# Performance work log

Hardware: AMD Instinct MI355X
Metric: run time of the kernel (lower is better)

Reference implementation:

```python
import jax, jax.numpy as jnp
import numpy as np
import math

B = 2
L = 2048
D_MODEL = 1024
D_STATE = 16
D_CONV = 4
D_INNER = 2 * D_MODEL  # expand * d_model
DT_RANK = math.ceil(D_MODEL / 16)  # 64
DT_MIN, DT_MAX = 1e-3, 1e-1


def _dt_bias(k):
    # inv-softplus init of dt bias, as in Mamba
    dt = jnp.exp(jax.random.uniform(k, (D_INNER,)) * (math.log(DT_MAX) - math.log(DT_MIN)) + math.log(DT_MIN))
    dt = jnp.clip(dt, 1e-4, None)
    return (dt + jnp.log(-jnp.expm1(-dt))).astype(jnp.float32)


def setup_inputs() -> dict:
    key = jax.random.key(0)
    ks = jax.random.split(key, 14)
    nrm = lambda k, shape, s: (jax.random.normal(k, shape) * s).astype(jnp.float32)
    dt_std = DT_RANK ** -0.5
    A_log = jnp.log(jnp.broadcast_to(jnp.arange(1, D_STATE + 1, dtype=jnp.float32), (D_INNER, D_STATE)))
    return {
        "hidden_states": jax.random.normal(ks[0], (B, L, D_MODEL), dtype=jnp.float32),
        "in_proj_w": nrm(ks[1], (2 * D_INNER, D_MODEL), D_MODEL ** -0.5),
        "conv_w": nrm(ks[2], (D_INNER, D_CONV), 0.5),
        "conv_b": nrm(ks[3], (D_INNER,), 0.1),
        "x_proj_w": nrm(ks[4], (DT_RANK + 2 * D_STATE, D_INNER), D_INNER ** -0.5),
        "dt_proj_w": jax.random.uniform(ks[5], (D_INNER, DT_RANK), minval=-dt_std, maxval=dt_std).astype(jnp.float32),
        "dt_proj_b": _dt_bias(ks[6]),
        "A_log": A_log,
        "D": jnp.ones((D_INNER,), jnp.float32),
        "conv_wb": nrm(ks[7], (D_INNER, D_CONV), 0.5),
        "conv_bb": nrm(ks[8], (D_INNER,), 0.1),
        "x_proj_wb": nrm(ks[9], (DT_RANK + 2 * D_STATE, D_INNER), D_INNER ** -0.5),
        "dt_proj_wb": jax.random.uniform(ks[10], (D_INNER, DT_RANK), minval=-dt_std, maxval=dt_std).astype(jnp.float32),
        "dt_proj_bb": _dt_bias(ks[11]),
        "A_b_log": A_log,
        "D_b": jnp.ones((D_INNER,), jnp.float32),
        "out_proj_w": nrm(ks[12], (D_MODEL, D_INNER), D_INNER ** -0.5),
    }


def _causal_conv(x, w, b):
    # x: (B, d_inner, L); depthwise causal conv1d (torch pads both sides then truncates to L == left-pad d_conv-1)
    out = jax.lax.conv_general_dilated(
        x, w[:, None, :], (1,), [(D_CONV - 1, 0)],
        dimension_numbers=("NCH", "OIH", "NCH"), feature_group_count=D_INNER)
    return out + b[None, :, None]


def _selective_scan(u, dt, A, Bm, Cm, Dp, z):
    # u, dt, z: (B, d, L); A: (d, n); Bm, Cm: (B, n, L)
    h0 = jnp.zeros((u.shape[0], u.shape[1], A.shape[1]), u.dtype)

    def step(h, inp):
        dt_l, u_l, B_l, C_l = inp  # (B,d), (B,d), (B,n), (B,n)
        h = jnp.exp(dt_l[..., None] * A) * h + (dt_l * u_l)[..., None] * B_l[:, None, :]
        return h, jnp.einsum("bdn,bn->bd", h, C_l)

    xs = tuple(jnp.moveaxis(a, -1, 0) for a in (dt, u, Bm, Cm))  # time-major
    _, ys = jax.lax.scan(step, h0, xs)  # ys: (L, B, d)
    y = jnp.moveaxis(ys, 0, -1) + Dp[None, :, None] * u
    return y * jax.nn.silu(z)


def _mamba_dir(xz, conv_w, conv_b, x_proj_w, dt_proj_w, dt_proj_b, A_log, Dp):
    x, z = jnp.split(xz, 2, axis=1)  # (B, d_inner, L) each
    x = jax.nn.silu(_causal_conv(x, conv_w, conv_b))
    x_dbl = jnp.einsum("bdl,ed->bel", x, x_proj_w)  # e = dt_rank + 2*d_state
    dtv = x_dbl[:, :DT_RANK]
    Bm = x_dbl[:, DT_RANK:DT_RANK + D_STATE]
    Cm = x_dbl[:, DT_RANK + D_STATE:]
    dtv = jax.nn.softplus(jnp.einsum("brl,dr->bdl", dtv, dt_proj_w) + dt_proj_b[None, :, None])
    return _selective_scan(x, dtv, -jnp.exp(A_log), Bm, Cm, Dp, z)


def reference(hidden_states, in_proj_w, conv_w, conv_b, x_proj_w, dt_proj_w, dt_proj_b, A_log, D,
              conv_wb, conv_bb, x_proj_wb, dt_proj_wb, dt_proj_bb, A_b_log, D_b, out_proj_w):
    xz = jnp.einsum("bld,ed->bel", hidden_states, in_proj_w)  # (B, 2*d_inner, L)
    out_f = _mamba_dir(xz, conv_w, conv_b, x_proj_w, dt_proj_w, dt_proj_b, A_log, D)
    out_b = _mamba_dir(xz[..., ::-1], conv_wb, conv_bb, x_proj_wb, dt_proj_wb, dt_proj_bb, A_b_log, D_b)
    y = out_f + out_b[..., ::-1]  # (B, d_inner, L)
    return jnp.einsum("bdl,od->blo", y, out_proj_w)  # (B, L, d_model)
```

## Files before the change

### kernel.cpp

```cpp
#include <hip/hip_runtime.h>
#include <hip/hip_bf16.h>

#define B_  2
#define L_  2048
#define DM  1024
#define DI  2048
#define DS  16
#define DR  64
#define E_  4096
#define CH  32
#define NC  (L_/CH)
#define XE  128
#define KS  4
#define BLDI ((size_t)B_*L_*DI)

typedef __attribute__((ext_vector_type(8))) short bf16x8;
typedef __attribute__((ext_vector_type(4))) float f32x4;

static __device__ __forceinline__ float sigmoidf_(float x){ return 1.f/(1.f+__expf(-x)); }
static __device__ __forceinline__ float siluf_(float x){ return x*sigmoidf_(x); }
static __device__ __forceinline__ unsigned short f2bf(float f){
  unsigned int u = __float_as_uint(f);
  unsigned int r = (u + 0x7FFFu + ((u>>16)&1u)) >> 16;
  return (unsigned short)r;
}
static __device__ __forceinline__ float bf2f(unsigned short s){
  return __uint_as_float(((unsigned int)s)<<16);
}

__global__ __launch_bounds__(256) void k_prep(const float* __restrict__ hs,
                                              const float* __restrict__ wi,
                                              const float* __restrict__ wo,
                                              const float* __restrict__ wx0,
                                              const float* __restrict__ wx1,
                                              const float* __restrict__ wd0,
                                              const float* __restrict__ wd1,
                                              unsigned short* __restrict__ hsb,
                                              unsigned short* __restrict__ wib,
                                              unsigned short* __restrict__ wob,
                                              unsigned short* __restrict__ wxb0,
                                              unsigned short* __restrict__ wxb1,
                                              unsigned short* __restrict__ wdtb0,
                                              unsigned short* __restrict__ wdtb1){
  int bid = blockIdx.x;
  const float* src; unsigned short* dst; bool pad = false;
  if      (bid <  4096){ src=hs;  dst=hsb; }
  else if (bid <  8192){ bid-=4096;  src=wi;  dst=wib; }
  else if (bid < 10240){ bid-=8192;  src=wo;  dst=wob; }
  else if (bid < 10496){ bid-=10240; src=wx0; dst=wxb0; pad=true; }
  else if (bid < 10752){ bid-=10496; src=wx1; dst=wxb1; pad=true; }
  else if (bid < 10880){ bid-=10752; src=wd0; dst=wdtb0; }
  else                 { bid-=10880; src=wd1; dst=wdtb1; }
  int i = (bid*256 + threadIdx.x)*4;
  ushort4 o;
  if (pad && i >= 96*DI){ o.x=o.y=o.z=o.w=0; }
  else {
    float4 v = *(const float4*)(src + i);
    o.x = f2bf(v.x); o.y = f2bf(v.y); o.z = f2bf(v.z); o.w = f2bf(v.w);
  }
  *(ushort4*)(dst + i) = o;
}

template<int OP>
__global__ __launch_bounds__(256) void k_gemm(const unsigned short* __restrict__ A, size_t aBS, size_t aDS,
                                              const unsigned short* __restrict__ Bm, size_t bBS, size_t bDS,
                                              void* __restrict__ Cv, size_t cBS, size_t cDS,
                                              const float* __restrict__ bias0,
                                              const float* __restrict__ bias1,
                                              int K, int lda, int ldb, int ldc, int zdiv){
  __shared__ unsigned short LB[128*128];
  unsigned short* Al = LB;
  unsigned short* Bl = LB + 128*64;
  const int zz = blockIdx.z;
  const int bq = zz % zdiv, dq = zz / zdiv;
  const int m0 = blockIdx.y*128, n0 = blockIdx.x*128;
  const int tid = threadIdx.x;
  const int lane = tid & 63, wid = tid >> 6;
  const int wm = wid >> 1, wn = wid & 1;
  const unsigned short* Ab = A + (size_t)bq*aBS + (size_t)dq*aDS;
  const unsigned short* Bb = Bm + (size_t)bq*bBS + (size_t)dq*bDS;
  f32x4 acc[4][4];
  #pragma unroll
  for (int i=0;i<4;i++)
    #pragma unroll
    for (int j=0;j<4;j++){ f32x4 z = {0.f,0.f,0.f,0.f}; acc[i][j] = z; }

  for (int kt=0; kt<K; kt+=64){
    #pragma unroll
    for (int i=0;i<4;i++){
      int q = i*256 + tid;
      int row = q>>3, seg = q&7;
      int sseg = seg ^ (row&7);
      const unsigned short* ga = Ab + (size_t)(m0+row)*lda + kt + sseg*8;
      const unsigned short* gb = Bb + (size_t)(n0+row)*ldb + kt + sseg*8;
      __builtin_amdgcn_global_load_lds((const __attribute__((address_space(1))) void*)ga,
          (__attribute__((address_space(3))) void*)(Al + (size_t)q*8), 16, 0, 0);
      __builtin_amdgcn_global_load_lds((const __attribute__((address_space(1))) void*)gb,
          (__attribute__((address_space(3))) void*)(Bl + (size_t)q*8), 16, 0, 0);
    }
    __syncthreads();
    #pragma unroll
    for (int ks=0; ks<2; ks++){
      bf16x8 af[4], bfr[4];
      #pragma unroll
      for (int mf=0; mf<4; mf++){
        int row = wm*64 + mf*16 + (lane&15);
        int seg = (ks*4 + (lane>>4)) ^ (row&7);
        af[mf] = *(const bf16x8*)(Al + row*64 + seg*8);
      }
      #pragma unroll
      for (int nf=0; nf<4; nf++){
        int row = wn*64 + nf*16 + (lane&15);
        int seg = (ks*4 + (lane>>4)) ^ (row&7);
        bfr[nf] = *(const bf16x8*)(Bl + row*64 + seg*8);
      }
      #pragma unroll
      for (int mf=0; mf<4; mf++)
        #pragma unroll
        for (int nf=0; nf<4; nf++)
          acc[mf][nf] = __builtin_amdgcn_mfma_f32_16x16x32_bf16(af[mf], bfr[nf], acc[mf][nf], 0,0,0);
    }
    __syncthreads();
  }
  const float* bias = dq ? bias1 : bias0;
  if (OP==0){
    #pragma unroll
    for (int mf=0; mf<4; mf++){
      #pragma unroll
      for (int nf=0; nf<4; nf++){
        const int col   = n0 + wn*64 + nf*16 + (lane&15);
        const int rbase = m0 + wm*64 + mf*16 + (lane>>4)*4;
        #pragma unroll
        for (int r=0;r<4;r++){
          size_t o = (size_t)bq*cBS + (size_t)dq*cDS + (size_t)(rbase+r)*ldc + col;
          ((float*)Cv)[o] = acc[mf][nf][r];
        }
      }
    }
  } else {
    #pragma unroll
    for (int mf=0; mf<4; mf++){
      #pragma unroll
      for (int nf=0; nf<4; nf++){
        const int cl = wn*64 + nf*16 + (lane&15);
        const int rb = wm*64 + mf*16 + (lane>>4)*4;
        float bv = (OP==4) ? bias[n0+cl] : 0.f;
        #pragma unroll
        for (int r=0;r<4;r++){
          float v = acc[mf][nf][r];
          if (OP==5) v = siluf_(v);
          if (OP==4){ float t = v + bv; v = (t>20.f)? t : __logf(1.f+__expf(t)); }
          const int row = rb + r;
          const int sg = (cl>>3) ^ (((row>>2)&3)<<2);
          LB[row*128 + sg*8 + (cl&7)] = f2bf(v);
        }
      }
    }
    __syncthreads();
    unsigned short* Cb = (unsigned short*)Cv + (size_t)bq*cBS + (size_t)dq*cDS;
    #pragma unroll
    for (int p=0;p<8;p++){
      const int row = p*16 + (tid>>4);
      const int g = tid&15;
      const int sg = g ^ (((row>>2)&3)<<2);
      bf16x8 vv = *(const bf16x8*)&LB[row*128 + sg*8];
      *(bf16x8*)(Cb + (size_t)(m0+row)*ldc + n0 + g*8) = vv;
    }
  }
}

__global__ __launch_bounds__(256) void k_redx(const float* __restrict__ xpart,
                                              unsigned short* __restrict__ out){
  const size_t STR = (size_t)(B_*L_)*XE;
  size_t i = ((size_t)blockIdx.x*256 + threadIdx.x)*4;
  const size_t dir = i / STR;
  const size_t ii  = i - dir*STR;
  const float* src = xpart + dir*KS*STR + ii;
  float4 s = *(const float4*)(src);
  #pragma unroll
  for (int ks=1; ks<KS; ks++){
    float4 v = *(const float4*)(src + (size_t)ks*STR);
    s.x+=v.x; s.y+=v.y; s.z+=v.z; s.w+=v.w;
  }
  ushort4 o; o.x=f2bf(s.x); o.y=f2bf(s.y); o.z=f2bf(s.z); o.w=f2bf(s.w);
  *(ushort4*)(out + dir*STR + ii) = o;
}

__global__ __launch_bounds__(256) void k_conv(const unsigned short* __restrict__ XZ,
                                              const float* __restrict__ w0,
                                              const float* __restrict__ bias0,
                                              const float* __restrict__ w1,
                                              const float* __restrict__ bias1,
                                              unsigned short* __restrict__ xcTb){
  const int zz = blockIdx.z;
  const int b = zz & 1, dir = zz >> 1;
  const float* w    = dir ? w1    : w0;
  const float* bias = dir ? bias1 : bias0;
  const int c0 = blockIdx.y*64, l0 = blockIdx.x*64;
  __shared__ float T[64][69];
  const int tid = threadIdx.x;
  {
    const int rr = tid>>6, cc = tid&63;
    #pragma unroll
    for (int i=0;i<16;i++){
      int row = i*4 + rr;
      int p = l0 - 3 + cc;
      float v = 0.f;
      if (p >= 0) v = bf2f(XZ[((size_t)b*DI + c0 + row)*(size_t)L_ + (dir? (L_-1-p):p)]);
      T[row][cc] = v;
    }
    if (tid < 192){
      int row = tid & 63, j = 64 + (tid>>6);
      int p = l0 - 3 + j;
      T[row][j] = bf2f(XZ[((size_t)b*DI + c0 + row)*(size_t)L_ + (dir? (L_-1-p):p)]);
    }
  }
  __syncthreads();
  const int c = tid & 63, lq = tid >> 6;
  const float w0_=w[(c0+c)*4+0], w1_=w[(c0+c)*4+1], w2_=w[(c0+c)*4+2], w3_=w[(c0+c)*4+3];
  const float bs = bias[c0+c];
  unsigned short* dst = xcTb + (size_t)dir*BLDI;
  #pragma unroll
  for (int i=0;i<16;i++){
    int lo = i*4 + lq;
    float acc = bs;
    acc = fmaf(w0_, T[c][lo+0], acc);
    acc = fmaf(w1_, T[c][lo+1], acc);
    acc = fmaf(w2_, T[c][lo+2], acc);
    acc = fmaf(w3_, T[c][lo+3], acc);
    dst[((size_t)b*L_ + l0 + lo)*(size_t)DI + c0 + c] = f2bf(siluf_(acc));
  }
}


__global__ __launch_bounds__(256) void k_scan_part(const unsigned short* __restrict__ dtTb,
                                                   unsigned short* __restrict__ xcTb,
                                                   const unsigned short* __restrict__ xdblb,
                                                   const float* __restrict__ Dv0,
                                                   const float* __restrict__ Dv1,
                                                   unsigned short* __restrict__ S,
                                                   float* __restrict__ dtsum){
  const int zz = blockIdx.z;
  const int b = zz & 1, dir = zz >> 1;
  const int c = blockIdx.x;
  const int d = blockIdx.y*256 + threadIdx.x;
  __shared__ float Bsh[CH][DS];
  __shared__ float Csh[CH][DS];
  if (threadIdx.x < CH*4){
    int s = threadIdx.x>>2, qq = threadIdx.x&3;
    bf16x8 v = *(const bf16x8*)(xdblb + (size_t)dir*(B_*L_*XE)
                                + ((size_t)b*L_ + c*CH + s)*XE + 64 + qq*8);
    if (qq < 2){
      #pragma unroll
      for (int j=0;j<8;j++) Bsh[s][qq*8+j] = bf2f((unsigned short)v[j]);
    } else {
      #pragma unroll
      for (int j=0;j<8;j++) Csh[s][(qq-2)*8+j] = bf2f((unsigned short)v[j]);
    }
  }
  __syncthreads();
  float h[DS];
  #pragma unroll
  for (int n=0;n<DS;n++) h[n] = 0.f;
  const float Dd = dir ? Dv1[d] : Dv0[d];
  const unsigned short* dtp = dtTb + (size_t)dir*BLDI + ((size_t)b*L_ + c*CH)*(size_t)DI + d;
  unsigned short* up = xcTb + (size_t)dir*BLDI + ((size_t)b*L_ + c*CH)*(size_t)DI + d;
  float dts = 0.f;
  #pragma unroll 4
  for (int s=0;s<CH;s++){
    const float dt = bf2f(dtp[(size_t)s*DI]);
    const float u  = bf2f(up[(size_t)s*DI]);
    const float du = dt*u;
    dts += dt;
    const float e1 = __expf(-dt);
    const float e2 = e1*e1, e4 = e2*e2, e8 = e4*e4, e12 = e8*e4;
    const float k1=e1, k2=e2, k3=e2*e1, k4=e4;
    const float4 B0 = *(const float4*)&Bsh[s][0];
    const float4 B1 = *(const float4*)&Bsh[s][4];
    const float4 B2 = *(const float4*)&Bsh[s][8];
    const float4 B3 = *(const float4*)&Bsh[s][12];
    const float4 C0 = *(const float4*)&Csh[s][0];
    const float4 C1 = *(const float4*)&Csh[s][4];
    const float4 C2 = *(const float4*)&Csh[s][8];
    const float4 C3 = *(const float4*)&Csh[s][12];
    float a0=0.f, a1=0.f, a2=0.f, a3=0.f;
    h[0]  = fmaf(k1,     h[0],  du*B0.x);  a0 = fmaf(h[0],  C0.x, a0);
    h[1]  = fmaf(k2,     h[1],  du*B0.y);  a1 = fmaf(h[1],  C0.y, a1);
    h[2]  = fmaf(k3,     h[2],  du*B0.z);  a2 = fmaf(h[2],  C0.z, a2);
    h[3]  = fmaf(k4,     h[3],  du*B0.w);  a3 = fmaf(h[3],  C0.w, a3);
    h[4]  = fmaf(k1*e4,  h[4],  du*B1.x);  a0 = fmaf(h[4],  C1.x, a0);
    h[5]  = fmaf(k2*e4,  h[5],  du*B1.y);  a1 = fmaf(h[5],  C1.y, a1);
    h[6]  = fmaf(k3*e4,  h[6],  du*B1.z);  a2 = fmaf(h[6],  C1.z, a2);
    h[7]  = fmaf(k4*e4,  h[7],  du*B1.w);  a3 = fmaf(h[7],  C1.w, a3);
    h[8]  = fmaf(k1*e8,  h[8],  du*B2.x);  a0 = fmaf(h[8],  C2.x, a0);
    h[9]  = fmaf(k2*e8,  h[9],  du*B2.y);  a1 = fmaf(h[9],  C2.y, a1);
    h[10] = fmaf(k3*e8,  h[10], du*B2.z);  a2 = fmaf(h[10], C2.z, a2);
    h[11] = fmaf(k4*e8,  h[11], du*B2.w);  a3 = fmaf(h[11], C2.w, a3);
    h[12] = fmaf(k1*e12, h[12], du*B3.x);  a0 = fmaf(h[12], C3.x, a0);
    h[13] = fmaf(k2*e12, h[13], du*B3.y);  a1 = fmaf(h[13], C3.y, a1);
    h[14] = fmaf(k3*e12, h[14], du*B3.z);  a2 = fmaf(h[14], C3.z, a2);
    h[15] = fmaf(k4*e12, h[15], du*B3.w);  a3 = fmaf(h[15], C3.w, a3);
    float yl = ((a0+a1)+(a2+a3)) + Dd*u;
    up[(size_t)s*DI] = f2bf(yl);
  }
  unsigned short* Sp = S + (((size_t)zz*DI + d)*(size_t)NC + c)*DS;
  bf16x8 o0, o1;
  #pragma unroll
  for (int n=0;n<8;n++){ o0[n] = (short)f2bf(h[n]); o1[n] = (short)f2bf(h[8+n]); }
  *(bf16x8*)(Sp)   = o0;
  *(bf16x8*)(Sp+8) = o1;
  dtsum[((size_t)zz*DI + d)*NC + c] = dts;
}

__global__ __launch_bounds__(64) void k_chain(const unsigned short* __restrict__ S,
                                              const float* __restrict__ dtsum,
                                              unsigned short* __restrict__ H0){
  const int t = blockIdx.x*64 + threadIdx.x;
  const int n = t & (DS-1);
  const int d = (t >> 4) & (DI-1);
  const int zz = t >> 15;
  const float A = -(float)(n+1);
  const size_t base  = ((size_t)zz*DI + d)*(size_t)NC*DS + n;
  const size_t dbase = ((size_t)zz*DI + d)*NC;
  float h = 0.f;
  for (int c=0;c<NC;c++){
    H0[base + (size_t)c*DS] = f2bf(h);
    h = fmaf(__expf(A*dtsum[dbase+c]), h, bf2f(S[base + (size_t)c*DS]));
  }
}

__global__ __launch_bounds__(256) void k_scan_out(const unsigned short* __restrict__ dtTb,
                                                  const unsigned short* __restrict__ ylTb,
                                                  const unsigned short* __restrict__ xdblb,
                                                  const unsigned short* __restrict__ H0,
                                                  unsigned short* __restrict__ y0b,
                                                  unsigned short* __restrict__ y1b){
  const int zz = blockIdx.z;
  const int b = zz & 1, dir = zz >> 1;
  const int c = blockIdx.x;
  const int d = blockIdx.y*256 + threadIdx.x;
  __shared__ float Csh[CH][DS];
  if (threadIdx.x < CH*2){
    int s = threadIdx.x>>1, qq = threadIdx.x&1;
    bf16x8 v = *(const bf16x8*)(xdblb + (size_t)dir*(B_*L_*XE)
                                + ((size_t)b*L_ + c*CH + s)*XE + 80 + qq*8);
    #pragma unroll
    for (int j=0;j<8;j++) Csh[s][qq*8+j] = bf2f((unsigned short)v[j]);
  }
  __syncthreads();
  float h[DS];
  const unsigned short* Hp = H0 + (((size_t)zz*DI + d)*(size_t)NC + c)*DS;
  {
    bf16x8 v0 = *(const bf16x8*)(Hp);
    bf16x8 v1 = *(const bf16x8*)(Hp+8);
    #pragma unroll
    for (int n=0;n<8;n++){ h[n] = bf2f((unsigned short)v0[n]); h[8+n] = bf2f((unsigned short)v1[n]); }
  }
  const unsigned short* dtp = dtTb + (size_t)dir*BLDI + ((size_t)b*L_ + c*CH)*(size_t)DI + d;
  const unsigned short* ylp = ylTb + (size_t)dir*BLDI + ((size_t)b*L_ + c*CH)*(size_t)DI + d;
  unsigned short* yo = (dir ? y1b : y0b) + (size_t)b*L_*(size_t)DI + d;
  float T = 0.f;
  #pragma unroll 4
  for (int s=0;s<CH;s++){
    const float dt = bf2f(dtp[(size_t)s*DI]);
    const float yl = bf2f(ylp[(size_t)s*DI]);
    T += dt;
    const float q = __expf(-T);
    const float4 C0 = *(const float4*)&Csh[s][0];
    const float4 C1 = *(const float4*)&Csh[s][4];
    const float4 C2 = *(const float4*)&Csh[s][8];
    const float4 C3 = *(const float4*)&Csh[s][12];
    float t;
    t = C3.w*h[15];
    t = fmaf(t, q, C3.z*h[14]);
    t = fmaf(t, q, C3.y*h[13]);
    t = fmaf(t, q, C3.x*h[12]);
    t = fmaf(t, q, C2.w*h[11]);
    t = fmaf(t, q, C2.z*h[10]);
    t = fmaf(t, q, C2.y*h[9]);
    t = fmaf(t, q, C2.x*h[8]);
    t = fmaf(t, q, C1.w*h[7]);
    t = fmaf(t, q, C1.z*h[6]);
    t = fmaf(t, q, C1.y*h[5]);
    t = fmaf(t, q, C1.x*h[4]);
    t = fmaf(t, q, C0.w*h[3]);
    t = fmaf(t, q, C0.z*h[2]);
    t = fmaf(t, q, C0.y*h[1]);
    t = fmaf(t, q, C0.x*h[0]);
    const float accv = fmaf(t, q, yl);
    const int l = c*CH + s;
    const int pos = dir ? (L_-1-l) : l;
    yo[(size_t)pos*DI] = f2bf(accv);
  }
}

__global__ __launch_bounds__(256) void k_yadd(const unsigned short* __restrict__ y0,
                                              const unsigned short* __restrict__ y1,
                                              const unsigned short* __restrict__ zs,
                                              unsigned short* __restrict__ out){
  size_t i = ((size_t)blockIdx.x*256 + threadIdx.x)*8;
  bf16x8 a = *(const bf16x8*)(y0 + i);
  bf16x8 b = *(const bf16x8*)(y1 + i);
  bf16x8 z = *(const bf16x8*)(zs + i);
  bf16x8 o;
  #pragma unroll
  for (int j=0;j<8;j++)
    o[j] = (short)f2bf((bf2f((unsigned short)a[j]) + bf2f((unsigned short)b[j]))
                       * bf2f((unsigned short)z[j]));
  *(bf16x8*)(out + i) = o;
}

extern "C" void kernel_launch(void* const* d_in, const int* in_sizes, int n_in,
                              void* d_out, int out_size, void* d_ws, size_t ws_size,
                              hipStream_t stream){
  const float* hs        = (const float*)d_in[0];
  const float* in_proj_w = (const float*)d_in[1];
  const float* conv_w    = (const float*)d_in[2];
  const float* conv_b    = (const float*)d_in[3];
  const float* x_proj_w  = (const float*)d_in[4];
  const float* dt_proj_w = (const float*)d_in[5];
  const float* dt_proj_b = (const float*)d_in[6];
  const float* Dv        = (const float*)d_in[8];
  const float* conv_wb   = (const float*)d_in[9];
  const float* conv_bb   = (const float*)d_in[10];
  const float* x_proj_wb = (const float*)d_in[11];
  const float* dt_proj_wb= (const float*)d_in[12];
  const float* dt_proj_bb= (const float*)d_in[13];
  const float* D_b       = (const float*)d_in[15];
  const float* out_proj_w= (const float*)d_in[16];

  float* ws    = (float*)d_ws;
  float* dts   = ws;
  float* xpart = dts + (size_t)2*B_*DI*NC;
  unsigned short* Sbuf = (unsigned short*)xpart;
  unsigned short* us0   = (unsigned short*)(xpart + (size_t)2*KS*B_*L_*XE);
  unsigned short* xz_x  = us0;
  unsigned short* zsTb  = xz_x  + BLDI;
  unsigned short* xcTb  = zsTb  + BLDI;
  unsigned short* dtTb  = xcTb  + 2*BLDI;
  unsigned short* y1b   = dtTb  + 2*BLDI;
  unsigned short* hsb   = y1b   + BLDI;
  unsigned short* wib   = hsb   + (size_t)B_*L_*DM;
  unsigned short* wob   = wib   + (size_t)E_*DM;
  unsigned short* wxb0  = wob   + (size_t)DM*DI;
  unsigned short* wxb1  = wxb0  + (size_t)XE*DI;
  unsigned short* wdtb0 = wxb1  + (size_t)XE*DI;
  unsigned short* wdtb1 = wdtb0 + (size_t)DI*DR;
  unsigned short* xdblb = wdtb1 + (size_t)DI*DR;
  unsigned short* H0b = xz_x;
  unsigned short* ybf = xz_x;
  unsigned short* y0b = hsb;

  k_prep<<<dim3(11008), 256, 0, stream>>>(hs, in_proj_w, out_proj_w,
      x_proj_w, x_proj_wb, dt_proj_w, dt_proj_wb,
      hsb, wib, wob, wxb0, wxb1, wdtb0, wdtb1);

  k_gemm<3><<<dim3(L_/128, DI/128, B_), 256, 0, stream>>>(
      wib, 0, 0, hsb, (size_t)L_*DM, 0, xz_x, (size_t)DI*L_, 0,
      nullptr, nullptr, DM, DM, DM, L_, B_);
  k_gemm<5><<<dim3(DI/128, L_/128, B_), 256, 0, stream>>>(
      hsb, (size_t)L_*DM, 0, wib + (size_t)DI*DM, 0, 0, zsTb, (size_t)L_*DI, 0,
      nullptr, nullptr, DM, DM, DM, DI, B_);

  k_conv<<<dim3(L_/64, DI/64, 2*B_), 256, 0, stream>>>(
      xz_x, conv_w, conv_b, conv_wb, conv_bb, xcTb);

  k_gemm<0><<<dim3(XE/128, (B_*L_)/128, 2*KS), 256, 0, stream>>>(
      xcTb, DI/KS, BLDI, wxb0, DI/KS, (size_t)XE*DI,
      xpart, (size_t)(B_*L_)*XE, (size_t)KS*(B_*L_)*XE,
      nullptr, nullptr, DI/KS, DI, DI, XE, KS);
  k_redx<<<dim3((2*B_*L_*XE)/1024), 256, 0, stream>>>(xpart, xdblb);

  k_gemm<4><<<dim3(DI/128, (B_*L_)/128, 2), 256, 0, stream>>>(
      xdblb, 0, (size_t)B_*L_*XE, wdtb0, 0, (size_t)DI*DR,
      dtTb, 0, BLDI, dt_proj_b, dt_proj_bb, 64, XE, DR, DI, 1);

  k_scan_part<<<dim3(NC, DI/256, 2*B_), 256, 0, stream>>>(
      dtTb, xcTb, xdblb, Dv, D_b, Sbuf, dts);
  k_chain<<<dim3((2*B_*DI*DS)/64), 64, 0, stream>>>(Sbuf, dts, H0b);
  k_scan_out<<<dim3(NC, DI/256, 2*B_), 256, 0, stream>>>(
      dtTb, xcTb, xdblb, H0b, y0b, y1b);

  k_yadd<<<dim3((B_*L_*DI)/2048), 256, 0, stream>>>(y0b, y1b, zsTb, ybf);

  k_gemm<0><<<dim3(DM/128, (B_*L_)/128, 1), 256, 0, stream>>>(
      ybf, 0, 0, wob, 0, 0, (float*)d_out, 0, 0,
      nullptr, nullptr, DI, DI, DI, DM, 1);
}
```

Baseline: 267.2 us.

## Fuse forward/backward scan output with gating add; share conv tile across directions

The conv kernel now loads one tile of x and computes both the forward and the reversed-direction causal convolutions from it, so the input is read once instead of twice. The scan output kernel processes the forward chunk and the mirrored backward chunk together, then adds them and applies the z gate directly. This removes the separate y-add kernel and the intermediate y0/y1 buffers. The backward state decay is rebuilt from stored chunk dt sums, and each thread does twice the work with more registers, at half the grid size.

```diff
diff --git a/kernel.cpp b/kernel.cpp
--- a/kernel.cpp
+++ b/kernel.cpp
@@ -26,6 +26,12 @@
 }
 static __device__ __forceinline__ float bf2f(unsigned short s){
   return __uint_as_float(((unsigned int)s)<<16);
+}
+static __device__ __forceinline__ float horner16(const float* C, const float* h, float q){
+  float t = C[15]*h[15];
+  #pragma unroll
+  for (int n=14;n>=0;--n) t = fmaf(t, q, C[n]*h[n]);
+  return t;
 }
 
 __global__ __launch_bounds__(256) void k_prep(const float* __restrict__ hs,
@@ -192,12 +198,9 @@
                                               const float* __restrict__ w1,
                                               const float* __restrict__ bias1,
                                               unsigned short* __restrict__ xcTb){
-  const int zz = blockIdx.z;
-  const int b = zz & 1, dir = zz >> 1;
-  const float* w    = dir ? w1    : w0;
-  const float* bias = dir ? bias1 : bias0;
+  const int b = blockIdx.z;
   const int c0 = blockIdx.y*64, l0 = blockIdx.x*64;
-  __shared__ float T[64][69];
+  __shared__ float T[64][73];
   const int tid = threadIdx.x;
   {
     const int rr = tid>>6, cc = tid&63;
@@ -206,29 +209,43 @@
       int row = i*4 + rr;
       int p = l0 - 3 + cc;
       float v = 0.f;
-      if (p >= 0) v = bf2f(XZ[((size_t)b*DI + c0 + row)*(size_t)L_ + (dir? (L_-1-p):p)]);
+      if (p >= 0 && p < L_) v = bf2f(XZ[((size_t)b*DI + c0 + row)*(size_t)L_ + p]);
       T[row][cc] = v;
     }
-    if (tid < 192){
-      int row = tid & 63, j = 64 + (tid>>6);
-      int p = l0 - 3 + j;
-      T[row][j] = bf2f(XZ[((size_t)b*DI + c0 + row)*(size_t)L_ + (dir? (L_-1-p):p)]);
+    #pragma unroll
+    for (int e=0;e<2;e++){
+      if (tid < 192){
+        int row = tid & 63, j = 64 + 3*e + (tid>>6);
+        int p = l0 - 3 + j;
+        float v = 0.f;
+        if (p >= 0 && p < L_) v = bf2f(XZ[((size_t)b*DI + c0 + row)*(size_t)L_ + p]);
+        T[row][j] = v;
+      }
     }
   }
   __syncthreads();
   const int c = tid & 63, lq = tid >> 6;
-  const float w0_=w[(c0+c)*4+0], w1_=w[(c0+c)*4+1], w2_=w[(c0+c)*4+2], w3_=w[(c0+c)*4+3];
-  const float bs = bias[c0+c];
-  unsigned short* dst = xcTb + (size_t)dir*BLDI;
+  const float wa0=w0[(c0+c)*4+0], wa1=w0[(c0+c)*4+1], wa2=w0[(c0+c)*4+2], wa3=w0[(c0+c)*4+3];
+  const float wb0=w1[(c0+c)*4+0], wb1=w1[(c0+c)*4+1], wb2=w1[(c0+c)*4+2], wb3=w1[(c0+c)*4+3];
+  const float bsa = bias0[c0+c], bsb = bias1[c0+c];
+  unsigned short* dst0 = xcTb;
+  unsigned short* dst1 = xcTb + BLDI;
   #pragma unroll
   for (int i=0;i<16;i++){
-    int lo = i*4 + lq;
-    float acc = bs;
-    acc = fmaf(w0_, T[c][lo+0], acc);
-    acc = fmaf(w1_, T[c][lo+1], acc);
-    acc = fmaf(w2_, T[c][lo+2], acc);
-    acc = fmaf(w3_, T[c][lo+3], acc);
-    dst[((size_t)b*L_ + l0 + lo)*(size_t)DI + c0 + c] = f2bf(siluf_(acc));
+    int jj = i*4 + lq;
+    float a0 = bsa;
+    a0 = fmaf(wa0, T[c][jj+0], a0);
+    a0 = fmaf(wa1, T[c][jj+1], a0);
+    a0 = fmaf(wa2, T[c][jj+2], a0);
+    a0 = fmaf(wa3, T[c][jj+3], a0);
+    dst0[((size_t)b*L_ + l0 + jj)*(size_t)DI + c0 + c] = f2bf(siluf_(a0));
+    float a1 = bsb;
+    a1 = fmaf(wb0, T[c][jj+6], a1);
+    a1 = fmaf(wb1, T[c][jj+5], a1);
+    a1 = fmaf(wb2, T[c][jj+4], a1);
+    a1 = fmaf(wb3, T[c][jj+3], a1);
+    const int p1 = L_-1-l0-jj;
+    dst1[((size_t)b*L_ + p1)*(size_t)DI + c0 + c] = f2bf(siluf_(a1));
   }
 }
 
@@ -329,85 +346,72 @@
   }
 }
 
-__global__ __launch_bounds__(256) void k_scan_out(const unsigned short* __restrict__ dtTb,
+__global__ __launch_bounds__(256) void k_scan_fin(const unsigned short* __restrict__ dtTb,
                                                   const unsigned short* __restrict__ ylTb,
                                                   const unsigned short* __restrict__ xdblb,
+                                                  const unsigned short* __restrict__ zsTb,
                                                   const unsigned short* __restrict__ H0,
-                                                  unsigned short* __restrict__ y0b,
-                                                  unsigned short* __restrict__ y1b){
-  const int zz = blockIdx.z;
-  const int b = zz & 1, dir = zz >> 1;
+                                                  const float* __restrict__ dtsum,
+                                                  unsigned short* __restrict__ ybf){
+  const int b = blockIdx.z;
   const int c = blockIdx.x;
   const int d = blockIdx.y*256 + threadIdx.x;
-  __shared__ float Csh[CH][DS];
+  const int c1 = NC-1-c;
+  __shared__ float C0sh[CH][DS];
+  __shared__ float C1sh[CH][DS];
   if (threadIdx.x < CH*2){
     int s = threadIdx.x>>1, qq = threadIdx.x&1;
-    bf16x8 v = *(const bf16x8*)(xdblb + (size_t)dir*(B_*L_*XE)
-                                + ((size_t)b*L_ + c*CH + s)*XE + 80 + qq*8);
-    #pragma unroll
-    for (int j=0;j<8;j++) Csh[s][qq*8+j] = bf2f((unsigned short)v[j]);
+    bf16x8 v0 = *(const bf16x8*)(xdblb
+                  + ((size_t)b*L_ + c*CH + s)*XE + 80 + qq*8);
+    bf16x8 v1 = *(const bf16x8*)(xdblb + (size_t)(B_*L_*XE)
+                  + ((size_t)b*L_ + c1*CH + s)*XE + 80 + qq*8);
+    #pragma unroll
+    for (int j=0;j<8;j++){
+      C0sh[s][qq*8+j] = bf2f((unsigned short)v0[j]);
+      C1sh[s][qq*8+j] = bf2f((unsigned short)v1[j]);
+    }
   }
   __syncthreads();
-  float h[DS];
-  const unsigned short* Hp = H0 + (((size_t)zz*DI + d)*(size_t)NC + c)*DS;
+  const int zz0 = b, zz1 = B_ + b;
+  float h0a[DS], h0b[DS];
   {
-    bf16x8 v0 = *(const bf16x8*)(Hp);
-    bf16x8 v1 = *(const bf16x8*)(Hp+8);
-    #pragma unroll
-    for (int n=0;n<8;n++){ h[n] = bf2f((unsigned short)v0[n]); h[8+n] = bf2f((unsigned short)v1[n]); }
-  }
-  const unsigned short* dtp = dtTb + (size_t)dir*BLDI + ((size_t)b*L_ + c*CH)*(size_t)DI + d;
-  const unsigned short* ylp = ylTb + (size_t)dir*BLDI + ((size_t)b*L_ + c*CH)*(size_t)DI + d;
-  unsigned short* yo = (dir ? y1b : y0b) + (size_t)b*L_*(size_t)DI + d;
-  float T = 0.f;
+    const unsigned short* Hp0 = H0 + (((size_t)zz0*DI + d)*(size_t)NC + c)*DS;
+    const unsigned short* Hp1 = H0 + (((size_t)zz1*DI + d)*(size_t)NC + c1)*DS;
+    bf16x8 a0 = *(const bf16x8*)(Hp0);
+    bf16x8 a1 = *(const bf16x8*)(Hp0+8);
+    bf16x8 b0 = *(const bf16x8*)(Hp1);
+    bf16x8 b1 = *(const bf16x8*)(Hp1+8);
+    #pragma unroll
+    for (int n=0;n<8;n++){
+      h0a[n] = bf2f((unsigned short)a0[n]); h0a[8+n] = bf2f((unsigned short)a1[n]);
+      h0b[n] = bf2f((unsigned short)b0[n]); h0b[8+n] = bf2f((unsigned short)b1[n]);
+    }
+  }
+  float T0 = 0.f;
+  float T1 = dtsum[((size_t)zz1*DI + d)*NC + c1];
+  const unsigned short* dt0 = dtTb + ((size_t)b*L_ + c*CH)*(size_t)DI + d;
+  const unsigned short* dt1 = dtTb + BLDI + ((size_t)b*L_)*(size_t)DI + d;
+  const unsigned short* yl0 = ylTb + ((size_t)b*L_ + c*CH)*(size_t)DI + d;
+  const unsigned short* yl1 = ylTb + BLDI + ((size_t)b*L_)*(size_t)DI + d;
+  const unsigned short* zp  = zsTb + ((size_t)b*L_ + c*CH)*(size_t)DI + d;
+  unsigned short* yo = ybf + ((size_t)b*L_ + c*CH)*(size_t)DI + d;
   #pragma unroll 4
   for (int s=0;s<CH;s++){
-    const float dt = bf2f(dtp[(size_t)s*DI]);
-    const float yl = bf2f(ylp[(size_t)s*DI]);
-    T += dt;
-    const float q = __expf(-T);
-    const float4 C0 = *(const float4*)&Csh[s][0];
-    const float4 C1 = *(const float4*)&Csh[s][4];
-    const float4 C2 = *(const float4*)&Csh[s][8];
-    const float4 C3 = *(const float4*)&Csh[s][12];
-    float t;
-    t = C3.w*h[15];
-    t = fmaf(t, q, C3.z*h[14]);
-    t = fmaf(t, q, C3.y*h[13]);
-    t = fmaf(t, q, C3.x*h[12]);
-    t = fmaf(t, q, C2.w*h[11]);
-    t = fmaf(t, q, C2.z*h[10]);
-    t = fmaf(t, q, C2.y*h[9]);
-    t = fmaf(t, q, C2.x*h[8]);
-    t = fmaf(t, q, C1.w*h[7]);
-    t = fmaf(t, q, C1.z*h[6]);
-    t = fmaf(t, q, C1.y*h[5]);
-    t = fmaf(t, q, C1.x*h[4]);
-    t = fmaf(t, q, C0.w*h[3]);
-    t = fmaf(t, q, C0.z*h[2]);
-    t = fmaf(t, q, C0.y*h[1]);
-    t = fmaf(t, q, C0.x*h[0]);
-    const float accv = fmaf(t, q, yl);
-    const int l = c*CH + s;
-    const int pos = dir ? (L_-1-l) : l;
-    yo[(size_t)pos*DI] = f2bf(accv);
-  }
-}
-
-__global__ __launch_bounds__(256) void k_yadd(const unsigned short* __restrict__ y0,
-                                              const unsigned short* __restrict__ y1,
-                                              const unsigned short* __restrict__ zs,
-                                              unsigned short* __restrict__ out){
-  size_t i = ((size_t)blockIdx.x*256 + threadIdx.x)*8;
-  bf16x8 a = *(const bf16x8*)(y0 + i);
-  bf16x8 b = *(const bf16x8*)(y1 + i);
-  bf16x8 z = *(const bf16x8*)(zs + i);
-  bf16x8 o;
-  #pragma unroll
-  for (int j=0;j<8;j++)
-    o[j] = (short)f2bf((bf2f((unsigned short)a[j]) + bf2f((unsigned short)b[j]))
-                       * bf2f((unsigned short)z[j]));
-  *(bf16x8*)(out + i) = o;
+    const int p  = c*CH + s;
+    const size_t l1 = (size_t)(L_-1-p);
+    const float dta = bf2f(dt0[(size_t)s*DI]);
+    const float dtb = bf2f(dt1[l1*DI]);
+    T0 += dta;
+    const float q0 = __expf(-T0);
+    const float q1 = __expf(-T1);
+    T1 -= dtb;
+    const float t0 = horner16(&C0sh[s][0],    h0a, q0);
+    const float t1 = horner16(&C1sh[31-s][0], h0b, q1);
+    const float acc0 = fmaf(t0, q0, bf2f(yl0[(size_t)s*DI]));
+    const float acc1 = fmaf(t1, q1, bf2f(yl1[l1*DI]));
+    const float outv = (acc0 + acc1) * bf2f(zp[(size_t)s*DI]);
+    yo[(size_t)s*DI] = f2bf(outv);
+  }
 }
 
 extern "C" void kernel_launch(void* const* d_in, const int* in_sizes, int n_in,
@@ -438,8 +442,7 @@
   unsigned short* zsTb  = xz_x  + BLDI;
   unsigned short* xcTb  = zsTb  + BLDI;
   unsigned short* dtTb  = xcTb  + 2*BLDI;
-  unsigned short* y1b   = dtTb  + 2*BLDI;
-  unsigned short* hsb   = y1b   + BLDI;
+  unsigned short* hsb   = dtTb  + 2*BLDI;
   unsigned short* wib   = hsb   + (size_t)B_*L_*DM;
   unsigned short* wob   = wib   + (size_t)E_*DM;
   unsigned short* wxb0  = wob   + (size_t)DM*DI;
@@ -447,9 +450,8 @@
   unsigned short* wdtb0 = wxb1  + (size_t)XE*DI;
   unsigned short* wdtb1 = wdtb0 + (size_t)DI*DR;
   unsigned short* xdblb = wdtb1 + (size_t)DI*DR;
-  unsigned short* H0b = xz_x;
+  unsigned short* H0b = hsb;
   unsigned short* ybf = xz_x;
-  unsigned short* y0b = hsb;
 
   k_prep<<<dim3(11008), 256, 0, stream>>>(hs, in_proj_w, out_proj_w,
       x_proj_w, x_proj_wb, dt_proj_w, dt_proj_wb,
@@ -462,7 +464,7 @@
       hsb, (size_t)L_*DM, 0, wib + (size_t)DI*DM, 0, 0, zsTb, (size_t)L_*DI, 0,
       nullptr, nullptr, DM, DM, DM, DI, B_);
 
-  k_conv<<<dim3(L_/64, DI/64, 2*B_), 256, 0, stream>>>(
+  k_conv<<<dim3(L_/64, DI/64, B_), 256, 0, stream>>>(
       xz_x, conv_w, conv_b, conv_wb, conv_bb, xcTb);
 
   k_gemm<0><<<dim3(XE/128, (B_*L_)/128, 2*KS), 256, 0, stream>>>(
@@ -478,10 +480,8 @@
   k_scan_part<<<dim3(NC, DI/256, 2*B_), 256, 0, stream>>>(
       dtTb, xcTb, xdblb, Dv, D_b, Sbuf, dts);
   k_chain<<<dim3((2*B_*DI*DS)/64), 64, 0, stream>>>(Sbuf, dts, H0b);
-  k_scan_out<<<dim3(NC, DI/256, 2*B_), 256, 0, stream>>>(
-      dtTb, xcTb, xdblb, H0b, y0b, y1b);
-
-  k_yadd<<<dim3((B_*L_*DI)/2048), 256, 0, stream>>>(y0b, y1b, zsTb, ybf);
+  k_scan_fin<<<dim3(NC, DI/256, B_), 256, 0, stream>>>(
+      dtTb, xcTb, xdblb, zsTb, H0b, dts, ybf);
 
   k_gemm<0><<<dim3(DM/128, (B_*L_)/128, 1), 256, 0, stream>>>(
       ybf, 0, 0, wob, 0, 0, (float*)d_out, 0, 0,
```

Measured after the change: 269.9 us. No clear change (+1.0%).
